# Performance work log

Measured on AMD Instinct MI355X. Metric: run time of the kernel, lower is better.

## Reference

```python
import math
import jax, jax.numpy as jnp
import numpy as np

B, S, D, H, HD = 32, 512, 768, 12, 64
K, ST = 2, 2  # pooling kernel / stride
NEG = jnp.float32(-10000.0)


def _alibi_slopes(n):
    def p2(m):
        start = 2 ** (-(2 ** (-(math.log2(m) - 3))))
        return [start * start ** i for i in range(m)]
    if math.log2(n).is_integer():
        return p2(n)
    c = 2 ** math.floor(math.log2(n))
    return p2(c) + _alibi_slopes(2 * c)[0::2][: n - c]


def _sum_pool(x, k, s, out_len):
    # x: [B, L, C]; ceil_mode sum-pool over axis 1 (zero padded on the right)
    pad = (out_len - 1) * s + k - x.shape[1]
    if pad > 0:
        x = jnp.pad(x, ((0, 0), (0, pad), (0, 0)))
    win = x[:, jnp.arange(out_len)[:, None] * s + jnp.arange(k)]  # [B, out, k, C]
    return win.sum(axis=2)


def setup_inputs() -> dict:
    key = jax.random.key(0)
    k1, k2, k3 = jax.random.split(key, 3)
    hidden_states = jax.random.normal(k1, (B, S, D), dtype=jnp.float32)
    lengths = jax.random.randint(k2, (B,), 128, S + 1)
    attention_mask = jnp.arange(S)[None, :] < lengths[:, None]  # bool [B,S]
    Wqkv_w = jax.random.normal(k3, (3 * D, D), dtype=jnp.float32) * 0.02
    Wqkv_b = jnp.zeros((3 * D,), dtype=jnp.float32)
    return {"hidden_states": hidden_states, "attention_mask": attention_mask,
            "Wqkv_w": Wqkv_w, "Wqkv_b": Wqkv_b}


def reference(hidden_states, attention_mask, Wqkv_w, Wqkv_b):
    b, s = attention_mask.shape
    qkv = hidden_states @ Wqkv_w.T + Wqkv_b  # [B,S,3D]
    qkv = qkv.reshape(b, s, 3, H, HD)        # '(t h d)' split order
    q = qkv[:, :, 0]                          # [B,S,H,HD]
    k = qkv[:, :, 1].transpose(0, 2, 1, 3)    # [B,H,S,HD]
    v = qkv[:, :, 2].transpose(0, 2, 1, 3)

    # MaskedAvgPool1d on queries (flattened heads), ceil_mode sum-pool / count
    kk = min(K, s)
    out_len = -(-(max(0, s - kk)) // ST) + 1
    q_flat = q.reshape(b, s, H * HD)
    q_flat = jnp.where(attention_mask[:, :, None], q_flat, 0.0)
    norm = _sum_pool(attention_mask.astype(jnp.float32)[:, :, None], kk, ST, out_len)  # [B,out,1]
    new_mask = norm[..., 0] != 0
    norm = jnp.where(norm == 0, 1.0, norm)
    q_pool = _sum_pool(q_flat, kk, ST, out_len) / norm  # [B,out,D]
    q = q_pool.reshape(b, out_len, H, HD).transpose(0, 2, 1, 3)  # [B,H,out,HD]

    # bias: 0 where (new_mask_q & mask_k), else -10000; plus ALiBi
    pair = new_mask[:, :, None] & attention_mask[:, None, :]  # [B,out,S]
    bias = jnp.where(pair, 0.0, NEG)[:, None, :, :]           # [B,1,out,S]
    rel = jnp.abs(jnp.arange(s)[None, :] - jnp.arange(out_len)[:, None])  # [out,S]
    slopes = jnp.asarray(_alibi_slopes(H), dtype=jnp.float32)
    alibi = slopes[:, None, None] * (-rel.astype(jnp.float32))  # [H,out,S]
    scores = jnp.einsum('bhqd,bhkd->bhqk', q, k) / math.sqrt(HD) + bias + alibi[None]
    attn = jax.nn.softmax(scores, axis=-1)
    out = jnp.einsum('bhqk,bhkd->bhqd', attn, v)  # [B,H,out,HD]
    out = out.transpose(0, 2, 1, 3).reshape(b, out_len, H * HD)
    return out, new_mask
```

## Files before the change

kernel.cpp:

```cpp
#include <hip/hip_runtime.h>

#define BB 32
#define SS 512
#define DD 768
#define HH 12
#define HDIM 64
#define OL 256
#define NQKV 2304
#define GM (BB*SS)

#define NEG2 (-14426.9504089f)

typedef __bf16 bf16_t;
typedef bf16_t bf16x8 __attribute__((ext_vector_type(8)));
typedef float f32x4 __attribute__((ext_vector_type(4)));
typedef unsigned short u16x8 __attribute__((ext_vector_type(8)));

__device__ __forceinline__ unsigned short f2bf(float f) {
  unsigned u = __float_as_uint(f);
  u = u + 0x7FFFu + ((u >> 16) & 1u);
  return (unsigned short)(u >> 16);
}
__device__ __forceinline__ float b2f(unsigned short s) {
  return __uint_as_float(((unsigned)s) << 16);
}

__global__ void conv_f32_bf16(const float* __restrict__ in,
                              unsigned short* __restrict__ out, int n4) {
  int i = blockIdx.x * blockDim.x + threadIdx.x;
  if (i >= n4) return;
  float4 v = ((const float4*)in)[i];
  ushort4 o;
  o.x = f2bf(v.x); o.y = f2bf(v.y); o.z = f2bf(v.z); o.w = f2bf(v.w);
  ((ushort4*)out)[i] = o;
}

__global__ void prep_mask(const void* __restrict__ mraw,
                          float* __restrict__ kbias,
                          float* __restrict__ invn,
                          unsigned char* __restrict__ nmask,
                          float* __restrict__ out_nm) {
  int b = blockIdx.x, t = threadIdx.x;
  const unsigned char* mb = (const unsigned char*)mraw;
  bool isbyte = (mb[1] != 0);
  int idx = b * SS + t;
  int mv = isbyte ? (int)(mb[idx] != 0) : (int)(((const int*)mraw)[idx] != 0);
  kbias[idx] = mv ? 0.f : NEG2;
  if (t < OL) {
    int i0 = b * SS + 2 * t, i1 = i0 + 1;
    int m0 = isbyte ? (int)(mb[i0] != 0) : (int)(((const int*)mraw)[i0] != 0);
    int m1 = isbyte ? (int)(mb[i1] != 0) : (int)(((const int*)mraw)[i1] != 0);
    int n = m0 + m1;
    invn[b * OL + t] = (n > 0) ? 1.f / (float)n : 1.f;
    nmask[b * OL + t] = (n > 0) ? 1 : 0;
    out_nm[b * OL + t] = (n > 0) ? 1.f : 0.f;
  }
}

__global__ void pool_conv(const float* __restrict__ hidden,
                          const float* __restrict__ kbias,
                          const float* __restrict__ invn,
                          unsigned short* __restrict__ Abf,
                          unsigned short* __restrict__ Apool) {
  int i = blockIdx.x * blockDim.x + threadIdx.x;
  if (i >= BB * OL * (DD / 4)) return;
  const int c = (i % 192) * 4;
  const int ol = i / 192;
  const int b = ol >> 8, o = ol & 255;
  const int s0 = b * SS + 2 * o;
  const float4 h0 = *(const float4*)(hidden + (size_t)s0 * DD + c);
  const float4 h1 = *(const float4*)(hidden + (size_t)(s0 + 1) * DD + c);
  ushort4 a0, a1, ap;
  a0.x = f2bf(h0.x); a0.y = f2bf(h0.y); a0.z = f2bf(h0.z); a0.w = f2bf(h0.w);
  a1.x = f2bf(h1.x); a1.y = f2bf(h1.y); a1.z = f2bf(h1.z); a1.w = f2bf(h1.w);
  const float m0v = (kbias[s0] == 0.f) ? 1.f : 0.f;
  const float m1v = (kbias[s0 + 1] == 0.f) ? 1.f : 0.f;
  const float inv = invn[ol];
  ap.x = f2bf((h0.x * m0v + h1.x * m1v) * inv);
  ap.y = f2bf((h0.y * m0v + h1.y * m1v) * inv);
  ap.z = f2bf((h0.z * m0v + h1.z * m1v) * inv);
  ap.w = f2bf((h0.w * m0v + h1.w * m1v) * inv);
  *(ushort4*)(Abf + (size_t)s0 * DD + c) = a0;
  *(ushort4*)(Abf + (size_t)(s0 + 1) * DD + c) = a1;
  *(ushort4*)(Apool + (size_t)ol * DD + c) = ap;
}

#define NT 12
__global__ __launch_bounds__(256, 2) void gemm_qkv(
    const unsigned short* __restrict__ A,
    const unsigned short* __restrict__ Apool,
    const unsigned short* __restrict__ Bt,
    const float* __restrict__ bias,
    unsigned short* __restrict__ Kbuf,
    unsigned short* __restrict__ qp,
    unsigned short* __restrict__ vT,
    const unsigned char* __restrict__ nmask) {
  __shared__ __align__(16) char smem[65536];

  const int t = threadIdx.x;
  const int lane = t & 63;
  const int w = t >> 6;
  const int wm = w >> 1, wn = w & 1;
  const int fr = lane & 15, hi = lane >> 4;

  const int p = blockIdx.x;
  const int l = (p & 7) * 240 + (p >> 3);
  const bool isQ = l >= 1536;
  int m0, n0;
  if (!isQ) { m0 = (l / 12) * 128; n0 = 768 + (l % 12) * 128; }
  else      { const int l2 = l - 1536; m0 = (l2 / 6) * 128; n0 = (l2 % 6) * 128; }
  const unsigned short* Asel = isQ ? Apool : A;

  f32x4 acc[4][4] = {};

  const int sr8 = lane >> 3;
  const int sx8 = ((lane & 7) ^ sr8) * 8;
  const int wq = __builtin_amdgcn_readfirstlane(w);
  const unsigned short* aSrc = Asel + (size_t)(m0 + wq * 32 + sr8) * DD + sx8;
  const unsigned short* bSrc = Bt + (size_t)(n0 + wq * 32 + sr8) * DD + sx8;

#define GLOAD(SRC, DST)                                                        \
  __builtin_amdgcn_global_load_lds(                                           \
      (const __attribute__((address_space(1))) unsigned int*)(SRC),           \
      (__attribute__((address_space(3))) unsigned int*)(DST), 16, 0, 0)

#define STAGE(T) do {                                                          \
    char* da_ = smem + ((T) & 1) * 32768;                                      \
    char* db_ = da_ + 16384;                                                   \
    const unsigned short* as_ = aSrc + (T) * 64;                               \
    const unsigned short* bs_ = bSrc + (T) * 64;                               \
    _Pragma("unroll")                                                          \
    for (int i_ = 0; i_ < 4; ++i_) {                                           \
      GLOAD(as_ + (size_t)i_ * 8 * DD, da_ + (wq * 32 + i_ * 8) * 128);        \
      GLOAD(bs_ + (size_t)i_ * 8 * DD, db_ + (wq * 32 + i_ * 8) * 128);        \
    }                                                                          \
  } while (0)

  STAGE(0);
  STAGE(1);

  const int cb0 = (hi * 16) ^ ((fr & 7) << 4);
  const int cb1 = (64 + hi * 16) ^ ((fr & 7) << 4);

  for (int kt = 0; kt < NT; ++kt) {
    if (kt < NT - 1) {
      asm volatile("s_waitcnt vmcnt(8)" ::: "memory");
    } else {
      asm volatile("s_waitcnt vmcnt(0)" ::: "memory");
    }
    __builtin_amdgcn_sched_barrier(0);
    __builtin_amdgcn_s_barrier();
    __builtin_amdgcn_sched_barrier(0);

    const char* bA = smem + (kt & 1) * 32768;
    const char* bB = bA + 16384;

    bf16x8 a0[4], b0[4], a1[4], b1[4];
#pragma unroll
    for (int f = 0; f < 4; ++f) {
      a0[f] = *(const bf16x8*)(bA + (wm * 64 + f * 16 + fr) * 128 + cb0);
      b0[f] = *(const bf16x8*)(bB + (wn * 64 + f * 16 + fr) * 128 + cb0);
    }
    __builtin_amdgcn_sched_barrier(0);
#pragma unroll
    for (int f = 0; f < 4; ++f) {
      a1[f] = *(const bf16x8*)(bA + (wm * 64 + f * 16 + fr) * 128 + cb1);
      b1[f] = *(const bf16x8*)(bB + (wn * 64 + f * 16 + fr) * 128 + cb1);
    }
    asm volatile("s_waitcnt lgkmcnt(8)" ::: "memory");
    __builtin_amdgcn_sched_barrier(0);
    __builtin_amdgcn_s_setprio(1);
#pragma unroll
    for (int mf = 0; mf < 4; ++mf)
#pragma unroll
      for (int nf = 0; nf < 4; ++nf)
        acc[mf][nf] = __builtin_amdgcn_mfma_f32_16x16x32_bf16(
            a0[mf], b0[nf], acc[mf][nf], 0, 0, 0);
    __builtin_amdgcn_s_setprio(0);
    asm volatile("s_waitcnt lgkmcnt(0)" ::: "memory");
    __builtin_amdgcn_sched_barrier(0);
    __builtin_amdgcn_s_barrier();
    __builtin_amdgcn_sched_barrier(0);
    if (kt + 2 < NT) STAGE(kt + 2);
    __builtin_amdgcn_sched_barrier(0);
    __builtin_amdgcn_s_setprio(1);
#pragma unroll
    for (int mf = 0; mf < 4; ++mf)
#pragma unroll
      for (int nf = 0; nf < 4; ++nf)
        acc[mf][nf] = __builtin_amdgcn_mfma_f32_16x16x32_bf16(
            a1[mf], b1[nf], acc[mf][nf], 0, 0, 0);
    __builtin_amdgcn_s_setprio(0);
  }
#undef STAGE
#undef GLOAD

  if (isQ) {
#pragma unroll
    for (int mf = 0; mf < 4; ++mf) {
      const int r0 = m0 + wm * 64 + mf * 16 + hi * 4;
      const uchar4 nm = *(const uchar4*)&nmask[r0];
      const float g0 = nm.x ? 1.f : 0.f;
      const float g1 = nm.y ? 1.f : 0.f;
      const float g2 = nm.z ? 1.f : 0.f;
      const float g3 = nm.w ? 1.f : 0.f;
#pragma unroll
      for (int nf = 0; nf < 4; ++nf) {
        const int gnc = n0 + wn * 64 + nf * 16 + fr;
        const float bvs = bias[gnc];
        const f32x4 a = acc[mf][nf];
        qp[(size_t)(r0 + 0) * 768 + gnc] = f2bf((a[0] + bvs) * g0);
        qp[(size_t)(r0 + 1) * 768 + gnc] = f2bf((a[1] + bvs) * g1);
        qp[(size_t)(r0 + 2) * 768 + gnc] = f2bf((a[2] + bvs) * g2);
        qp[(size_t)(r0 + 3) * 768 + gnc] = f2bf((a[3] + bvs) * g3);
      }
    }
  } else if (n0 < 1536) {
#pragma unroll
    for (int nf = 0; nf < 4; ++nf) {
      const int nc = wn * 64 + nf * 16 + fr;
      const float bvs = bias[n0 + nc];
      const int gnc = n0 - 768 + nc;
#pragma unroll
      for (int mf = 0; mf < 4; ++mf) {
        const int gmr = m0 + wm * 64 + mf * 16 + hi * 4;
#pragma unroll
        for (int j = 0; j < 4; ++j)
          Kbuf[(size_t)(gmr + j) * 768 + gnc] = f2bf(acc[mf][nf][j] + bvs);
      }
    }
  } else {
    const int b = m0 >> 9;
    const int s0 = m0 & 511;
    unsigned short* lt = (unsigned short*)smem;
#pragma unroll
    for (int nf = 0; nf < 4; ++nf) {
      const int nl = wn * 64 + nf * 16 + fr;
      const float bvs = bias[n0 + nl];
#pragma unroll
      for (int mf = 0; mf < 4; ++mf) {
        const int mb = wm * 64 + mf * 16 + hi * 4;
        ushort4 pk;
        pk.x = f2bf(acc[mf][nf][0] + bvs);
        pk.y = f2bf(acc[mf][nf][1] + bvs);
        pk.z = f2bf(acc[mf][nf][2] + bvs);
        pk.w = f2bf(acc[mf][nf][3] + bvs);
        *(ushort4*)&lt[nl * 136 + mb] = pk;
      }
    }
    __syncthreads();
#pragma unroll
    for (int i = 0; i < 8; ++i) {
      const int row = i * 16 + (t >> 4);
      const int ch = t & 15;
      const u16x8 v = *(const u16x8*)&lt[row * 136 + ch * 8];
      const int n = n0 - 1536 + row;
      const int h2 = n >> 6, d2 = n & 63;
      *(u16x8*)(vT + ((size_t)((b * HH + h2) * HDIM + d2)) * 512 + s0 + ch * 8) = v;
    }
  }
}

__constant__ float c_slopes2[12] = {
    0.72134752f, 0.36067376f, 0.18033688f, 0.09016844f,
    0.04508422f, 0.02254211f, 0.011271055f, 0.0056355275f,
    1.02013945f, 0.51006972f, 0.25503486f, 0.12751743f};

__global__ __launch_bounds__(256) void attn_mfma(
    const unsigned short* __restrict__ qp,
    const unsigned short* __restrict__ Kb,
    const unsigned short* __restrict__ vT,
    const float* __restrict__ kbias,
    const unsigned char* __restrict__ nmask,
    float* __restrict__ out) {
  __shared__ __align__(16) char smem[51200];
  const int t = threadIdx.x;
  const int lane = t & 63;
  const int w = t >> 6;
  const int wq = __builtin_amdgcn_readfirstlane(w);
  const int fr = lane & 15, hi = lane >> 4;

  const int p = blockIdx.x;
  const int l = (p & 7) * 96 + (p >> 3);
  const int qb = l & 1;
  const int bh = l >> 1;
  const int h = bh % HH, b = bh / HH;
  const int q0 = qb * 128 + wq * 32;

  char* ptb = smem + 32768 + wq * 4096;
  float* kbl = (float*)(smem + 49152);

  const int srow = lane >> 3;
  const int scol = ((lane & 7) ^ srow) * 8;

#define GLOAD(SRC, DST)                                                        \
  __builtin_amdgcn_global_load_lds(                                           \
      (const __attribute__((address_space(1))) unsigned int*)(SRC),           \
      (__attribute__((address_space(3))) unsigned int*)(DST), 16, 0, 0)

  if (wq == 0) {
    GLOAD(kbias + b * SS + lane * 4, smem + 49152);
    GLOAD(kbias + b * SS + 256 + lane * 4, smem + 50176);
  }

  bf16x8 qf[2][2];
#pragma unroll
  for (int m = 0; m < 2; ++m)
#pragma unroll
    for (int ks = 0; ks < 2; ++ks)
      qf[m][ks] = *(const bf16x8*)(qp + (size_t)(b * OL + q0 + m * 16 + fr) * DD +
                                   h * HDIM + ks * 32 + hi * 8);

  int nmv = (int)nmask[b * OL + q0 + (lane & 31)];
  int qmbits = 0;
#pragma unroll
  for (int m = 0; m < 2; ++m)
#pragma unroll
    for (int j = 0; j < 4; ++j)
      if (__shfl(nmv, m * 16 + hi * 4 + j, 64)) qmbits |= 1 << (m * 4 + j);

  const float slope2 = c_slopes2[h];
  f32x4 oacc[2][4] = {};
  float lpart[2][4] = {};

#define STAGE(TILE, BUF) do {                                                  \
    char* kd_ = smem + (BUF) * 8192 + wq * 2048;                               \
    char* vd_ = smem + 16384 + (BUF) * 8192 + wq * 2048;                       \
    const unsigned short* ks_ =                                                \
        Kb + (size_t)(b * SS + (TILE) * 64 + wq * 16 + srow) * 768 + h * HDIM + scol; \
    const unsigned short* vs_ =                                                \
        vT + (size_t)((b * HH + h) * HDIM + wq * 16 + srow) * SS + (TILE) * 64 + scol; \
    GLOAD(ks_, kd_);                                                           \
    GLOAD(ks_ + (size_t)8 * 768, kd_ + 1024);                                  \
    GLOAD(vs_, vd_);                                                           \
    GLOAD(vs_ + (size_t)8 * SS, vd_ + 1024);                                   \
  } while (0)

  __builtin_amdgcn_sched_barrier(0);
  STAGE(0, 0);
  STAGE(1, 1);
  __builtin_amdgcn_sched_barrier(0);

  for (int tile = 0; tile < 8; ++tile) {
    const int cur = tile & 1;
    const int key0 = tile * 64;
    if (tile < 7) {
      asm volatile("s_waitcnt vmcnt(4)" ::: "memory");
    } else {
      asm volatile("s_waitcnt vmcnt(0)" ::: "memory");
    }
    __builtin_amdgcn_sched_barrier(0);
    __builtin_amdgcn_s_barrier();
    __builtin_amdgcn_sched_barrier(0);

    char* ktb = smem + cur * 8192;
    char* vtb = smem + 16384 + cur * 8192;

    f32x4 sacc[2][4] = {};
#pragma unroll
    for (int ks = 0; ks < 2; ++ks) {
      bf16x8 kf[4];
#pragma unroll
      for (int n = 0; n < 4; ++n) {
        const int by = ((n * 16 + fr) * 128 + (ks * 64 + hi * 16)) ^ ((fr & 7) << 4);
        kf[n] = *(const bf16x8*)(ktb + by);
      }
#pragma unroll
      for (int m = 0; m < 2; ++m)
#pragma unroll
        for (int n = 0; n < 4; ++n)
          sacc[m][n] = __builtin_amdgcn_mfma_f32_16x16x32_bf16(qf[m][ks], kf[n], sacc[m][n], 0, 0, 0);
    }

    float kbv[4], keyfv[4];
#pragma unroll
    for (int n = 0; n < 4; ++n) {
      kbv[n] = kbl[key0 + n * 16 + fr];
      keyfv[n] = (float)(key0 + n * 16 + fr);
    }
#pragma unroll
    for (int m = 0; m < 2; ++m) {
#pragma unroll
      for (int j = 0; j < 4; ++j) {
        const bool qm = (qmbits >> (m * 4 + j)) & 1;
        const float qvf = (float)(q0 + m * 16 + hi * 4 + j);
        float lp = lpart[m][j];
#pragma unroll
        for (int n = 0; n < 4; ++n) {
          const float biasv = qm ? kbv[n] : 0.f;
          const float rel = fabsf(keyfv[n] - qvf);
          float tv = fmaf(sacc[m][n][j], 0.18033688011f, biasv);
          tv = fmaf(rel, -slope2, tv);
          float pe;
          asm("v_exp_f32 %0, %1" : "=v"(pe) : "v"(tv));
          lp += pe;
          const int by = ((m * 16 + hi * 4 + j) * 128 + (n * 16 + fr) * 2) ^
                         (((hi * 4 + j) & 7) << 4);
          *(unsigned short*)(ptb + by) = f2bf(pe);
        }
        lpart[m][j] = lp;
      }
    }
    asm volatile("s_waitcnt lgkmcnt(0)" ::: "memory");
    __builtin_amdgcn_sched_barrier(0);

#pragma unroll
    for (int ks = 0; ks < 2; ++ks) {
      bf16x8 pf[2], vf[4];
#pragma unroll
      for (int m = 0; m < 2; ++m) {
        const int by = ((m * 16 + fr) * 128 + (ks * 64 + hi * 16)) ^ ((fr & 7) << 4);
        pf[m] = *(const bf16x8*)(ptb + by);
      }
#pragma unroll
      for (int nd = 0; nd < 4; ++nd) {
        const int by = ((nd * 16 + fr) * 128 + (ks * 64 + hi * 16)) ^ ((fr & 7) << 4);
        vf[nd] = *(const bf16x8*)(vtb + by);
      }
#pragma unroll
      for (int m = 0; m < 2; ++m)
#pragma unroll
        for (int nd = 0; nd < 4; ++nd)
          oacc[m][nd] = __builtin_amdgcn_mfma_f32_16x16x32_bf16(pf[m], vf[nd], oacc[m][nd], 0, 0, 0);
    }

    __builtin_amdgcn_sched_barrier(0);
    __builtin_amdgcn_s_barrier();
    __builtin_amdgcn_sched_barrier(0);
    if (tile + 2 < 8) STAGE(tile + 2, cur);
  }
#undef STAGE
#undef GLOAD

  float* ot = (float*)(smem + wq * 8704);
#pragma unroll
  for (int m = 0; m < 2; ++m)
#pragma unroll
    for (int j = 0; j < 4; ++j) {
      float lv = lpart[m][j];
      lv += __shfl_xor(lv, 1, 64);
      lv += __shfl_xor(lv, 2, 64);
      lv += __shfl_xor(lv, 4, 64);
      lv += __shfl_xor(lv, 8, 64);
      const float rl = 1.f / lv;
      const int row = m * 16 + hi * 4 + j;
#pragma unroll
      for (int nd = 0; nd < 4; ++nd)
        ot[row * 68 + nd * 16 + fr] = oacc[m][nd][j] * rl;
    }
  asm volatile("s_waitcnt lgkmcnt(0)" ::: "memory");
  __builtin_amdgcn_sched_barrier(0);
#pragma unroll
  for (int i = 0; i < 8; ++i) {
    const int idx = i * 64 + lane;
    const int row = idx >> 4, c4 = idx & 15;
    const float4 v = *(const float4*)&ot[row * 68 + c4 * 4];
    *(float4*)(out + (size_t)(b * OL + q0 + row) * DD + h * HDIM + c4 * 4) = v;
  }
}

extern "C" void kernel_launch(void* const* d_in, const int* in_sizes, int n_in,
                              void* d_out, int out_size, void* d_ws, size_t ws_size,
                              hipStream_t stream) {
  const float* hidden = (const float*)d_in[0];
  const void* maskraw = d_in[1];
  const float* W = (const float*)d_in[2];
  const float* bias = (const float*)d_in[3];
  float* out = (float*)d_out;

  char* ws = (char*)d_ws;
  unsigned short* Abf   = (unsigned short*)(ws);
  unsigned short* Btb   = (unsigned short*)(ws + 25165824);
  unsigned short* Kbuf  = (unsigned short*)(ws + 28704768);
  unsigned short* vT    = (unsigned short*)(ws + 53870592);
  unsigned short* qp    = (unsigned short*)(ws + 79036416);
  float* kbias          = (float*)(ws + 91619328);
  float* invn           = (float*)(ws + 91684864);
  unsigned char* nmask  = (unsigned char*)(ws + 91717632);
  unsigned short* Apool = (unsigned short*)(ws + 91725824);

  float* out_nm = out + (size_t)BB * OL * DD;

  conv_f32_bf16<<<(NQKV * DD / 4 + 255) / 256, 256, 0, stream>>>(W, Btb, NQKV * DD / 4);
  prep_mask<<<BB, SS, 0, stream>>>(maskraw, kbias, invn, nmask, out_nm);
  pool_conv<<<(BB * OL * (DD / 4) + 255) / 256, 256, 0, stream>>>(hidden, kbias, invn, Abf, Apool);
  gemm_qkv<<<1920, 256, 0, stream>>>(Abf, Apool, Btb, bias, Kbuf, qp, vT, nmask);
  attn_mfma<<<768, 256, 0, stream>>>(qp, Kbuf, vT, kbias, nmask, out);
}
```

Baseline: 107.3 us.

## Fuse prep kernels into one launch and split attention across eight waves

Merges the weight conversion, mask preparation and pooling/convert kernels into a single kernel that picks its role by block index. The pooling branch now reads the raw mask directly, so it no longer depends on kbias being written first. The attention kernel moves from 256 to 512 threads per block, with each wave handling 16 query rows instead of 32, which halves per-wave registers and staging loads. The aim is to cut launch overhead and raise parallelism inside attention, at the cost of less reuse of K/V fragments per wave.

```diff
diff --git a/kernel.cpp b/kernel.cpp
--- a/kernel.cpp
+++ b/kernel.cpp
@@ -25,64 +25,67 @@
   return __uint_as_float(((unsigned)s) << 16);
 }
 
-__global__ void conv_f32_bf16(const float* __restrict__ in,
-                              unsigned short* __restrict__ out, int n4) {
-  int i = blockIdx.x * blockDim.x + threadIdx.x;
-  if (i >= n4) return;
-  float4 v = ((const float4*)in)[i];
-  ushort4 o;
-  o.x = f2bf(v.x); o.y = f2bf(v.y); o.z = f2bf(v.z); o.w = f2bf(v.w);
-  ((ushort4*)out)[i] = o;
-}
-
-__global__ void prep_mask(const void* __restrict__ mraw,
-                          float* __restrict__ kbias,
-                          float* __restrict__ invn,
-                          unsigned char* __restrict__ nmask,
-                          float* __restrict__ out_nm) {
-  int b = blockIdx.x, t = threadIdx.x;
+__global__ __launch_bounds__(256) void prep_all(
+    const float* __restrict__ hidden,
+    const void* __restrict__ mraw,
+    const float* __restrict__ W,
+    unsigned short* __restrict__ Btb,
+    unsigned short* __restrict__ Abf,
+    unsigned short* __restrict__ Apool,
+    float* __restrict__ kbias,
+    float* __restrict__ invn,
+    unsigned char* __restrict__ nmask,
+    float* __restrict__ out_nm) {
+  const int blk = blockIdx.x;
+  const int t = threadIdx.x;
   const unsigned char* mb = (const unsigned char*)mraw;
-  bool isbyte = (mb[1] != 0);
-  int idx = b * SS + t;
-  int mv = isbyte ? (int)(mb[idx] != 0) : (int)(((const int*)mraw)[idx] != 0);
-  kbias[idx] = mv ? 0.f : NEG2;
-  if (t < OL) {
-    int i0 = b * SS + 2 * t, i1 = i0 + 1;
-    int m0 = isbyte ? (int)(mb[i0] != 0) : (int)(((const int*)mraw)[i0] != 0);
-    int m1 = isbyte ? (int)(mb[i1] != 0) : (int)(((const int*)mraw)[i1] != 0);
-    int n = m0 + m1;
-    invn[b * OL + t] = (n > 0) ? 1.f / (float)n : 1.f;
-    nmask[b * OL + t] = (n > 0) ? 1 : 0;
-    out_nm[b * OL + t] = (n > 0) ? 1.f : 0.f;
-  }
-}
-
-__global__ void pool_conv(const float* __restrict__ hidden,
-                          const float* __restrict__ kbias,
-                          const float* __restrict__ invn,
-                          unsigned short* __restrict__ Abf,
-                          unsigned short* __restrict__ Apool) {
-  int i = blockIdx.x * blockDim.x + threadIdx.x;
-  if (i >= BB * OL * (DD / 4)) return;
-  const int c = (i % 192) * 4;
-  const int ol = i / 192;
-  const int b = ol >> 8, o = ol & 255;
-  const int s0 = b * SS + 2 * o;
-  const float4 h0 = *(const float4*)(hidden + (size_t)s0 * DD + c);
-  const float4 h1 = *(const float4*)(hidden + (size_t)(s0 + 1) * DD + c);
-  ushort4 a0, a1, ap;
-  a0.x = f2bf(h0.x); a0.y = f2bf(h0.y); a0.z = f2bf(h0.z); a0.w = f2bf(h0.w);
-  a1.x = f2bf(h1.x); a1.y = f2bf(h1.y); a1.z = f2bf(h1.z); a1.w = f2bf(h1.w);
-  const float m0v = (kbias[s0] == 0.f) ? 1.f : 0.f;
-  const float m1v = (kbias[s0 + 1] == 0.f) ? 1.f : 0.f;
-  const float inv = invn[ol];
-  ap.x = f2bf((h0.x * m0v + h1.x * m1v) * inv);
-  ap.y = f2bf((h0.y * m0v + h1.y * m1v) * inv);
-  ap.z = f2bf((h0.z * m0v + h1.z * m1v) * inv);
-  ap.w = f2bf((h0.w * m0v + h1.w * m1v) * inv);
-  *(ushort4*)(Abf + (size_t)s0 * DD + c) = a0;
-  *(ushort4*)(Abf + (size_t)(s0 + 1) * DD + c) = a1;
-  *(ushort4*)(Apool + (size_t)ol * DD + c) = ap;
+
+  if (blk < 1728) {
+    const int i = blk * 256 + t;
+    float4 v = ((const float4*)W)[i];
+    ushort4 o;
+    o.x = f2bf(v.x); o.y = f2bf(v.y); o.z = f2bf(v.z); o.w = f2bf(v.w);
+    ((ushort4*)Btb)[i] = o;
+  } else if (blk < 1792) {
+    const int idx = (blk - 1728) * 256 + t;
+    const int b = idx >> 9, s = idx & 511;
+    const bool isbyte = (mb[1] != 0);
+    const int mv = isbyte ? (int)(mb[idx] != 0) : (int)(((const int*)mraw)[idx] != 0);
+    kbias[idx] = mv ? 0.f : NEG2;
+    if (s < OL) {
+      const int i0 = b * SS + 2 * s, i1 = i0 + 1;
+      const int m0 = isbyte ? (int)(mb[i0] != 0) : (int)(((const int*)mraw)[i0] != 0);
+      const int m1 = isbyte ? (int)(mb[i1] != 0) : (int)(((const int*)mraw)[i1] != 0);
+      const int n = m0 + m1;
+      invn[b * OL + s] = (n > 0) ? 1.f / (float)n : 1.f;
+      nmask[b * OL + s] = (n > 0) ? 1 : 0;
+      out_nm[b * OL + s] = (n > 0) ? 1.f : 0.f;
+    }
+  } else {
+    const int i = (blk - 1792) * 256 + t;
+    const int c = (i % 192) * 4;
+    const int ol = i / 192;
+    const int b = ol >> 8, o = ol & 255;
+    const int s0 = b * SS + 2 * o;
+    const bool isbyte = (mb[1] != 0);
+    const int m0 = isbyte ? (int)(mb[s0] != 0) : (int)(((const int*)mraw)[s0] != 0);
+    const int m1 = isbyte ? (int)(mb[s0 + 1] != 0) : (int)(((const int*)mraw)[s0 + 1] != 0);
+    const int n = m0 + m1;
+    const float inv = (n > 0) ? 1.f / (float)n : 1.f;
+    const float m0v = (float)m0, m1v = (float)m1;
+    const float4 h0 = *(const float4*)(hidden + (size_t)s0 * DD + c);
+    const float4 h1 = *(const float4*)(hidden + (size_t)(s0 + 1) * DD + c);
+    ushort4 a0, a1, ap;
+    a0.x = f2bf(h0.x); a0.y = f2bf(h0.y); a0.z = f2bf(h0.z); a0.w = f2bf(h0.w);
+    a1.x = f2bf(h1.x); a1.y = f2bf(h1.y); a1.z = f2bf(h1.z); a1.w = f2bf(h1.w);
+    ap.x = f2bf((h0.x * m0v + h1.x * m1v) * inv);
+    ap.y = f2bf((h0.y * m0v + h1.y * m1v) * inv);
+    ap.z = f2bf((h0.z * m0v + h1.z * m1v) * inv);
+    ap.w = f2bf((h0.w * m0v + h1.w * m1v) * inv);
+    *(ushort4*)(Abf + (size_t)s0 * DD + c) = a0;
+    *(ushort4*)(Abf + (size_t)(s0 + 1) * DD + c) = a1;
+    *(ushort4*)(Apool + (size_t)ol * DD + c) = ap;
+  }
 }
 
 #define NT 12
@@ -266,7 +269,7 @@
     0.04508422f, 0.02254211f, 0.011271055f, 0.0056355275f,
     1.02013945f, 0.51006972f, 0.25503486f, 0.12751743f};
 
-__global__ __launch_bounds__(256) void attn_mfma(
+__global__ __launch_bounds__(512, 4) void attn_mfma(
     const unsigned short* __restrict__ qp,
     const unsigned short* __restrict__ Kb,
     const unsigned short* __restrict__ vT,
@@ -285,9 +288,9 @@
   const int qb = l & 1;
   const int bh = l >> 1;
   const int h = bh % HH, b = bh / HH;
-  const int q0 = qb * 128 + wq * 32;
-
-  char* ptb = smem + 32768 + wq * 4096;
+  const int q0 = qb * 128 + wq * 16;
+
+  char* ptb = smem + 32768 + wq * 2048;
   float* kbl = (float*)(smem + 49152);
 
   const int srow = lane >> 3;
@@ -303,37 +306,31 @@
     GLOAD(kbias + b * SS + 256 + lane * 4, smem + 50176);
   }
 
-  bf16x8 qf[2][2];
-#pragma unroll
-  for (int m = 0; m < 2; ++m)
-#pragma unroll
-    for (int ks = 0; ks < 2; ++ks)
-      qf[m][ks] = *(const bf16x8*)(qp + (size_t)(b * OL + q0 + m * 16 + fr) * DD +
-                                   h * HDIM + ks * 32 + hi * 8);
-
-  int nmv = (int)nmask[b * OL + q0 + (lane & 31)];
+  bf16x8 qf[2];
+#pragma unroll
+  for (int ks = 0; ks < 2; ++ks)
+    qf[ks] = *(const bf16x8*)(qp + (size_t)(b * OL + q0 + fr) * DD +
+                              h * HDIM + ks * 32 + hi * 8);
+
+  int nmv = (int)nmask[b * OL + q0 + (lane & 15)];
   int qmbits = 0;
 #pragma unroll
-  for (int m = 0; m < 2; ++m)
-#pragma unroll
-    for (int j = 0; j < 4; ++j)
-      if (__shfl(nmv, m * 16 + hi * 4 + j, 64)) qmbits |= 1 << (m * 4 + j);
+  for (int j = 0; j < 4; ++j)
+    if (__shfl(nmv, hi * 4 + j, 64)) qmbits |= 1 << j;
 
   const float slope2 = c_slopes2[h];
-  f32x4 oacc[2][4] = {};
-  float lpart[2][4] = {};
+  f32x4 oacc[4] = {};
+  float lpart[4] = {};
 
 #define STAGE(TILE, BUF) do {                                                  \
-    char* kd_ = smem + (BUF) * 8192 + wq * 2048;                               \
-    char* vd_ = smem + 16384 + (BUF) * 8192 + wq * 2048;                       \
+    char* kd_ = smem + (BUF) * 8192 + wq * 1024;                               \
+    char* vd_ = smem + 16384 + (BUF) * 8192 + wq * 1024;                       \
     const unsigned short* ks_ =                                                \
-        Kb + (size_t)(b * SS + (TILE) * 64 + wq * 16 + srow) * 768 + h * HDIM + scol; \
+        Kb + (size_t)(b * SS + (TILE) * 64 + wq * 8 + srow) * 768 + h * HDIM + scol; \
     const unsigned short* vs_ =                                                \
-        vT + (size_t)((b * HH + h) * HDIM + wq * 16 + srow) * SS + (TILE) * 64 + scol; \
+        vT + (size_t)((b * HH + h) * HDIM + wq * 8 + srow) * SS + (TILE) * 64 + scol; \
     GLOAD(ks_, kd_);                                                           \
-    GLOAD(ks_ + (size_t)8 * 768, kd_ + 1024);                                  \
     GLOAD(vs_, vd_);                                                           \
-    GLOAD(vs_ + (size_t)8 * SS, vd_ + 1024);                                   \
   } while (0)
 
   __builtin_amdgcn_sched_barrier(0);
@@ -345,7 +342,7 @@
     const int cur = tile & 1;
     const int key0 = tile * 64;
     if (tile < 7) {
-      asm volatile("s_waitcnt vmcnt(4)" ::: "memory");
+      asm volatile("s_waitcnt vmcnt(2)" ::: "memory");
     } else {
       asm volatile("s_waitcnt vmcnt(0)" ::: "memory");
     }
@@ -356,7 +353,7 @@
     char* ktb = smem + cur * 8192;
     char* vtb = smem + 16384 + cur * 8192;
 
-    f32x4 sacc[2][4] = {};
+    f32x4 sacc[4] = {};
 #pragma unroll
     for (int ks = 0; ks < 2; ++ks) {
       bf16x8 kf[4];
@@ -366,10 +363,8 @@
         kf[n] = *(const bf16x8*)(ktb + by);
       }
 #pragma unroll
-      for (int m = 0; m < 2; ++m)
-#pragma unroll
-        for (int n = 0; n < 4; ++n)
-          sacc[m][n] = __builtin_amdgcn_mfma_f32_16x16x32_bf16(qf[m][ks], kf[n], sacc[m][n], 0, 0, 0);
+      for (int n = 0; n < 4; ++n)
+        sacc[n] = __builtin_amdgcn_mfma_f32_16x16x32_bf16(qf[ks], kf[n], sacc[n], 0, 0, 0);
     }
 
     float kbv[4], keyfv[4];
@@ -379,38 +374,34 @@
       keyfv[n] = (float)(key0 + n * 16 + fr);
     }
 #pragma unroll
-    for (int m = 0; m < 2; ++m) {
-#pragma unroll
-      for (int j = 0; j < 4; ++j) {
-        const bool qm = (qmbits >> (m * 4 + j)) & 1;
-        const float qvf = (float)(q0 + m * 16 + hi * 4 + j);
-        float lp = lpart[m][j];
-#pragma unroll
-        for (int n = 0; n < 4; ++n) {
-          const float biasv = qm ? kbv[n] : 0.f;
-          const float rel = fabsf(keyfv[n] - qvf);
-          float tv = fmaf(sacc[m][n][j], 0.18033688011f, biasv);
-          tv = fmaf(rel, -slope2, tv);
-          float pe;
-          asm("v_exp_f32 %0, %1" : "=v"(pe) : "v"(tv));
-          lp += pe;
-          const int by = ((m * 16 + hi * 4 + j) * 128 + (n * 16 + fr) * 2) ^
-                         (((hi * 4 + j) & 7) << 4);
-          *(unsigned short*)(ptb + by) = f2bf(pe);
-        }
-        lpart[m][j] = lp;
-      }
+    for (int j = 0; j < 4; ++j) {
+      const bool qm = (qmbits >> j) & 1;
+      const float qvf = (float)(q0 + hi * 4 + j);
+      float lp = lpart[j];
+#pragma unroll
+      for (int n = 0; n < 4; ++n) {
+        const float biasv = qm ? kbv[n] : 0.f;
+        const float rel = fabsf(keyfv[n] - qvf);
+        float tv = fmaf(sacc[n][j], 0.18033688011f, biasv);
+        tv = fmaf(rel, -slope2, tv);
+        float pe;
+        asm("v_exp_f32 %0, %1" : "=v"(pe) : "v"(tv));
+        lp += pe;
+        const int by = ((hi * 4 + j) * 128 + (n * 16 + fr) * 2) ^
+                       (((hi * 4 + j) & 7) << 4);
+        *(unsigned short*)(ptb + by) = f2bf(pe);
+      }
+      lpart[j] = lp;
     }
     asm volatile("s_waitcnt lgkmcnt(0)" ::: "memory");
     __builtin_amdgcn_sched_barrier(0);
 
 #pragma unroll
     for (int ks = 0; ks < 2; ++ks) {
-      bf16x8 pf[2], vf[4];
-#pragma unroll
-      for (int m = 0; m < 2; ++m) {
-        const int by = ((m * 16 + fr) * 128 + (ks * 64 + hi * 16)) ^ ((fr & 7) << 4);
-        pf[m] = *(const bf16x8*)(ptb + by);
+      bf16x8 pf, vf[4];
+      {
+        const int by = (fr * 128 + (ks * 64 + hi * 16)) ^ ((fr & 7) << 4);
+        pf = *(const bf16x8*)(ptb + by);
       }
 #pragma unroll
       for (int nd = 0; nd < 4; ++nd) {
@@ -418,10 +409,8 @@
         vf[nd] = *(const bf16x8*)(vtb + by);
       }
 #pragma unroll
-      for (int m = 0; m < 2; ++m)
-#pragma unroll
-        for (int nd = 0; nd < 4; ++nd)
-          oacc[m][nd] = __builtin_amdgcn_mfma_f32_16x16x32_bf16(pf[m], vf[nd], oacc[m][nd], 0, 0, 0);
+      for (int nd = 0; nd < 4; ++nd)
+        oacc[nd] = __builtin_amdgcn_mfma_f32_16x16x32_bf16(pf, vf[nd], oacc[nd], 0, 0, 0);
     }
 
     __builtin_amdgcn_sched_barrier(0);
@@ -432,26 +421,24 @@
 #undef STAGE
 #undef GLOAD
 
-  float* ot = (float*)(smem + wq * 8704);
-#pragma unroll
-  for (int m = 0; m < 2; ++m)
-#pragma unroll
-    for (int j = 0; j < 4; ++j) {
-      float lv = lpart[m][j];
-      lv += __shfl_xor(lv, 1, 64);
-      lv += __shfl_xor(lv, 2, 64);
-      lv += __shfl_xor(lv, 4, 64);
-      lv += __shfl_xor(lv, 8, 64);
-      const float rl = 1.f / lv;
-      const int row = m * 16 + hi * 4 + j;
-#pragma unroll
-      for (int nd = 0; nd < 4; ++nd)
-        ot[row * 68 + nd * 16 + fr] = oacc[m][nd][j] * rl;
-    }
+  float* ot = (float*)(smem + wq * 4352);
+#pragma unroll
+  for (int j = 0; j < 4; ++j) {
+    float lv = lpart[j];
+    lv += __shfl_xor(lv, 1, 64);
+    lv += __shfl_xor(lv, 2, 64);
+    lv += __shfl_xor(lv, 4, 64);
+    lv += __shfl_xor(lv, 8, 64);
+    const float rl = 1.f / lv;
+    const int row = hi * 4 + j;
+#pragma unroll
+    for (int nd = 0; nd < 4; ++nd)
+      ot[row * 68 + nd * 16 + fr] = oacc[nd][j] * rl;
+  }
   asm volatile("s_waitcnt lgkmcnt(0)" ::: "memory");
   __builtin_amdgcn_sched_barrier(0);
 #pragma unroll
-  for (int i = 0; i < 8; ++i) {
+  for (int i = 0; i < 4; ++i) {
     const int idx = i * 64 + lane;
     const int row = idx >> 4, c4 = idx & 15;
     const float4 v = *(const float4*)&ot[row * 68 + c4 * 4];
@@ -481,9 +468,8 @@
 
   float* out_nm = out + (size_t)BB * OL * DD;
 
-  conv_f32_bf16<<<(NQKV * DD / 4 + 255) / 256, 256, 0, stream>>>(W, Btb, NQKV * DD / 4);
-  prep_mask<<<BB, SS, 0, stream>>>(maskraw, kbias, invn, nmask, out_nm);
-  pool_conv<<<(BB * OL * (DD / 4) + 255) / 256, 256, 0, stream>>>(hidden, kbias, invn, Abf, Apool);
+  prep_all<<<7936, 256, 0, stream>>>(hidden, maskraw, W, Btb, Abf, Apool,
+                                     kbias, invn, nmask, out_nm);
   gemm_qkv<<<1920, 256, 0, stream>>>(Abf, Apool, Btb, bias, Kbuf, qp, vT, nmask);
-  attn_mfma<<<768, 256, 0, stream>>>(qp, Kbuf, vT, kbias, nmask, out);
-}
+  attn_mfma<<<768, 512, 0, stream>>>(qp, Kbuf, vT, kbias, nmask, out);
+}
```

Result: faster. 96.62 us, median of 3 (-10.0%).
